# Performance work log

Hardware: AMD Instinct MI355X
Metric: run time of the kernel (lower is better)

The kernel has to match this reference:

```python
import jax, jax.numpy as jnp
import numpy as np
import math

DIM = 2048
NUM_HEADS = 16
HEAD_DIM = 128
SEQ = 2048
BATCH = 2
THETA = 10000.0


def _rope_freqs(seq_len, head_dim, theta=THETA):
    half = head_dim // 2
    inv = 1.0 / (theta ** (np.arange(0, half, dtype=np.float32) / half))
    t = np.arange(seq_len, dtype=np.float32)
    ang = np.outer(t, inv)  # [S, half]
    return jnp.asarray(np.cos(ang)), jnp.asarray(np.sin(ang))


def setup_inputs() -> dict:
    key = jax.random.key(0)
    ks = jax.random.split(key, 5)
    s = 1.0 / math.sqrt(DIM)
    cos, sin = _rope_freqs(SEQ, HEAD_DIM)
    return {
        "x": jax.random.normal(ks[0], (BATCH, SEQ, DIM), dtype=jnp.float32),
        "wq": jax.random.normal(ks[1], (DIM, NUM_HEADS * HEAD_DIM), dtype=jnp.float32) * s,
        "wk": jax.random.normal(ks[2], (DIM, NUM_HEADS * HEAD_DIM), dtype=jnp.float32) * s,
        "wv": jax.random.normal(ks[3], (DIM, NUM_HEADS * HEAD_DIM), dtype=jnp.float32) * s,
        "wo": jax.random.normal(ks[4], (NUM_HEADS * HEAD_DIM, DIM), dtype=jnp.float32) * s,
        "freqs_cos": cos,
        "freqs_sin": sin,
    }


def _apply_rope(x, cos, sin):
    # x: [B, S, H, Hd]; cos/sin: [S, Hd//2]
    B, S, H, Hd = x.shape
    xr = x.astype(jnp.float32).reshape(B, S, H, Hd // 2, 2)
    x0, x1 = xr[..., 0], xr[..., 1]
    c = cos[:S][None, :, None, :]
    sn = sin[:S][None, :, None, :]
    o0 = x0 * c - x1 * sn
    o1 = x0 * sn + x1 * c
    return jnp.stack([o0, o1], axis=-1).reshape(B, S, H, Hd)


def reference(x, wq, wk, wv, wo, freqs_cos, freqs_sin):
    B, S, D = x.shape
    H, Hd = NUM_HEADS, HEAD_DIM
    q = (x @ wq).reshape(B, S, H, Hd)
    k = (x @ wk).reshape(B, S, H, Hd)
    v = (x @ wv).reshape(B, S, H, Hd)
    q = _apply_rope(q, freqs_cos, freqs_sin)
    k = _apply_rope(k, freqs_cos, freqs_sin)
    # [B, H, S, S] causal attention scores
    scores = jnp.einsum("bqhd,bkhd->bhqk", q, k) / math.sqrt(Hd)
    causal = jnp.tril(jnp.ones((S, S), dtype=bool))
    scores = jnp.where(causal[None, None], scores, -jnp.inf)
    probs = jax.nn.softmax(scores.astype(jnp.float32), axis=-1)
    o = jnp.einsum("bhqk,bkhd->bqhd", probs, v).reshape(B, S, H * Hd)
    return o @ wo
```

## Files before the change

### kernel.cpp

```cpp
#include <hip/hip_runtime.h>
#include <hip/hip_bf16.h>

typedef __bf16 bf16;
typedef __attribute__((ext_vector_type(8))) __bf16 bf16x8;
typedef __attribute__((ext_vector_type(4))) __bf16 bf16x4;
typedef __attribute__((ext_vector_type(4))) float  f32x4;

typedef const void __attribute__((address_space(1)))* gas_t;
typedef void __attribute__((address_space(3)))* las_t;

__device__ __forceinline__ void gload16(const void* g, void* l) {
  __builtin_amdgcn_global_load_lds((gas_t)g, (las_t)l, 16, 0, 0);
}
__device__ __forceinline__ f32x4 mfma16(bf16x8 a, bf16x8 b, f32x4 c) {
  return __builtin_amdgcn_mfma_f32_16x16x32_bf16(a, b, c, 0, 0, 0);
}

constexpr int SEQL = 2048;
constexpr int DM   = 2048;
constexpr int HD   = 128;
constexpr int MR   = 4096;

__global__ __launch_bounds__(256) void cvt_x(const float* __restrict__ x,
                                             bf16* __restrict__ xb) {
  const size_t i = ((size_t)blockIdx.x * 256 + threadIdx.x) * 4;
  const f32x4 v = *reinterpret_cast<const f32x4*>(x + i);
  bf16x4 o;
  #pragma unroll
  for (int j = 0; j < 4; ++j) o[j] = (bf16)v[j];
  *reinterpret_cast<bf16x4*>(xb + i) = o;
}

__global__ __launch_bounds__(256) void transpose_w(
    const float* __restrict__ w0, const float* __restrict__ w1,
    const float* __restrict__ w2, const float* __restrict__ w3,
    bf16* __restrict__ wqkvt, bf16* __restrict__ wot) {
  const int z = blockIdx.z;
  const float* src = (z == 0) ? w0 : (z == 1) ? w1 : (z == 2) ? w2 : w3;
  bf16* dst = (z < 3) ? (wqkvt + (size_t)z * DM * DM) : wot;
  __shared__ float tile[32][33];
  const int tx = threadIdx.x, ty = threadIdx.y;
  const int x0 = blockIdx.x * 32, y0 = blockIdx.y * 32;
  #pragma unroll
  for (int i = 0; i < 4; ++i)
    tile[ty + 8 * i][tx] = src[(size_t)(y0 + ty + 8 * i) * DM + x0 + tx];
  __syncthreads();
  #pragma unroll
  for (int i = 0; i < 4; ++i)
    dst[(size_t)(x0 + ty + 8 * i) * DM + y0 + tx] = (bf16)tile[tx][ty + 8 * i];
}

__global__ __launch_bounds__(256) void rope_k(bf16* __restrict__ Q,
                                              bf16* __restrict__ Kk,
                                              const float* __restrict__ fc,
                                              const float* __restrict__ fs) {
  bf16* X = blockIdx.y ? Kk : Q;
  const size_t tid = (size_t)blockIdx.x * 256 + threadIdx.x;
  const size_t e0 = tid * 8;
  const int col = (int)(e0 & (DM - 1));
  const int row = (int)(e0 >> 11);
  const int s   = row & (SEQL - 1);
  const int p0  = (col & (HD - 1)) >> 1;
  bf16x8 v = *reinterpret_cast<bf16x8*>(X + e0);
  const f32x4 c  = *reinterpret_cast<const f32x4*>(fc + (size_t)s * 64 + p0);
  const f32x4 sn = *reinterpret_cast<const f32x4*>(fs + (size_t)s * 64 + p0);
  #pragma unroll
  for (int j = 0; j < 4; ++j) {
    const float x0 = (float)v[2 * j], x1 = (float)v[2 * j + 1];
    v[2 * j]     = (bf16)(x0 * c[j] - x1 * sn[j]);
    v[2 * j + 1] = (bf16)(x0 * sn[j] + x1 * c[j]);
  }
  *reinterpret_cast<bf16x8*>(X + e0) = v;
}

#define GPH(Q, STAGE, TAIL)                                                    \
  {                                                                            \
    const char* ap = aB + ((Q) * 32 + lo) * 128;                               \
    const bf16x8 a00 = *(const bf16x8*)(ap + su0);                             \
    const bf16x8 a01 = *(const bf16x8*)(ap + su1);                             \
    const bf16x8 a10 = *(const bf16x8*)(ap + 2048 + su0);                      \
    const bf16x8 a11 = *(const bf16x8*)(ap + 2048 + su1);                      \
    STAGE                                                                      \
    __builtin_amdgcn_s_barrier();                                              \
    asm volatile("s_waitcnt lgkmcnt(0)" ::: "memory");                         \
    __builtin_amdgcn_s_setprio(1);                                             \
    _Pragma("unroll")                                                          \
    for (int nf = 0; nf < 4; ++nf) {                                           \
      acc[2 * (Q)][nf]     = mfma16(a00, bfr[nf][0], acc[2 * (Q)][nf]);        \
      acc[2 * (Q)][nf]     = mfma16(a01, bfr[nf][1], acc[2 * (Q)][nf]);        \
      acc[2 * (Q) + 1][nf] = mfma16(a10, bfr[nf][0], acc[2 * (Q) + 1][nf]);    \
      acc[2 * (Q) + 1][nf] = mfma16(a11, bfr[nf][1], acc[2 * (Q) + 1][nf]);    \
    }                                                                          \
    __builtin_amdgcn_s_setprio(0);                                             \
    TAIL                                                                       \
    __builtin_amdgcn_s_barrier();                                              \
    asm volatile("" ::: "memory");                                             \
  }

template <bool MULTI>
__global__ __launch_bounds__(512, 2) void gemm8(
    const bf16* __restrict__ A, const bf16* __restrict__ Bt,
    bf16* __restrict__ Cb, const int M, const int N, const int K) {
  __shared__ __attribute__((aligned(16))) char lds[131072];
  const int t = threadIdx.x;
  const int wid = t >> 6, lane = t & 63, lo = lane & 15, hi = lane >> 4;
  const int wm = wid >> 2, wn = wid & 3;

  const int bid = blockIdx.x;
  const int nx = bid & 7;
  const int my = MULTI ? ((bid >> 3) & 15) : (bid >> 3);
  const int z  = MULTI ? (bid >> 7) : 0;
  const int m0 = my * 256, n0 = nx * 256;
  const bf16* Bt_ = Bt + (MULTI ? (size_t)z * N * K : 0);
  bf16* Cb_ = Cb + (MULTI ? (size_t)z * M * N : 0);

  const int urow  = (wid << 3) + (lane >> 3);
  const int uunit = (lane & 7) ^ ((lane >> 3) & 7);
  const bf16* gA = A   + (size_t)(m0 + urow) * K + uunit * 8;
  const bf16* gB = Bt_ + (size_t)(n0 + urow) * K + uunit * 8;
  char* lw = lds + wid * 1024;

  const int NT = K >> 6;

  auto stg = [&](const bf16* gbase, int buf, int op, int h, int kt) {
    const bf16* g = gbase + (size_t)(h * 128) * K + kt * 64;
    char* l = lw + (((buf << 1) | op) * 2 + h) * 16384;
    gload16(g, l);
    gload16(g + (size_t)64 * K, l + 8192);
  };
  auto stB0 = [&](int kt2) { stg(gB, kt2 & 1, 1, 0, kt2); };
  auto stB1 = [&](int kt2) { stg(gB, kt2 & 1, 1, 1, kt2); };
  auto stA0 = [&](int kt2) { stg(gA, kt2 & 1, 0, 0, kt2); };
  auto stA1 = [&](int kt2) { stg(gA, kt2 & 1, 0, 1, kt2); };

  f32x4 acc[8][4];
  #pragma unroll
  for (int i = 0; i < 8; ++i)
    #pragma unroll
    for (int j = 0; j < 4; ++j) acc[i][j] = (f32x4){0.f, 0.f, 0.f, 0.f};

  const int su0 = (hi ^ (lo & 7)) * 16;
  const int su1 = ((4 + hi) ^ (lo & 7)) * 16;

  stB0(0); stB1(0); stA0(0); stA1(0);
  stB0(1); stB1(1); stA0(1);
  asm volatile("s_waitcnt vmcnt(6)" ::: "memory");
  __builtin_amdgcn_s_barrier();
  asm volatile("" ::: "memory");

  #pragma unroll 1
  for (int kt = 0; kt < NT; ++kt) {
    const int bufc = kt & 1;
    const char* aB = lds + ((bufc * 2 + 0) * 2 + wm) * 16384;
    const char* bB = lds + ((bufc * 2 + 1) * 2 + (wn >> 1)) * 16384;
    bf16x8 bfr[4][2];
    {
      const char* bp = bB + ((wn & 1) * 64 + lo) * 128;
      #pragma unroll
      for (int nf = 0; nf < 4; ++nf) {
        bfr[nf][0] = *(const bf16x8*)(bp + nf * 2048 + su0);
        bfr[nf][1] = *(const bf16x8*)(bp + nf * 2048 + su1);
      }
    }
    GPH(0, if (kt + 1 < NT) stA1(kt + 1);, )
    GPH(1, if (kt + 2 < NT) stB0(kt + 2);, )
    GPH(2, if (kt + 2 < NT) stB1(kt + 2);, )
    GPH(3, if (kt + 2 < NT) stA0(kt + 2);,
        if (kt + 2 < NT) { asm volatile("s_waitcnt vmcnt(6)" ::: "memory"); }
        else             { asm volatile("s_waitcnt vmcnt(0)" ::: "memory"); })
  }

  #pragma unroll
  for (int mf = 0; mf < 8; ++mf)
    #pragma unroll
    for (int nf = 0; nf < 4; ++nf)
      #pragma unroll
      for (int r = 0; r < 4; ++r) {
        const size_t row = m0 + wm * 128 + mf * 16 + hi * 4 + r;
        const size_t col = n0 + wn * 64 + nf * 16 + lo;
        Cb_[row * N + col] = (bf16)acc[mf][nf][r];
      }
}

__global__ __launch_bounds__(256) void gemm_bt_f32(
    const bf16* __restrict__ A, const bf16* __restrict__ Bt,
    float* __restrict__ Cf, const int M, const int N, const int K) {
  const int t = threadIdx.x;
  const int wid = t >> 6, lane = t & 63, lo = lane & 15, hi = lane >> 4;
  const int m0 = blockIdx.y * 128, n0 = blockIdx.x * 128;
  __shared__ bf16 As[128 * 32];
  __shared__ bf16 Bs[128 * 32];
  const int wr = wid >> 1, wc = wid & 1;
  const f32x4 zero4 = {0.f, 0.f, 0.f, 0.f};
  f32x4 acc[4][4];
  #pragma unroll
  for (int i = 0; i < 4; ++i)
    #pragma unroll
    for (int j = 0; j < 4; ++j) acc[i][j] = zero4;

  const int r_a = t >> 2;
  const int ul  = ((t & 3) ^ (r_a & 3)) * 8;
  const bf16* gA0 = A  + (size_t)(m0 + r_a) * K + ul;
  const bf16* gB0 = Bt + (size_t)(n0 + r_a) * K + ul;
  char* lA = (char*)As + wid * 1024;
  char* lB = (char*)Bs + wid * 1024;

  const int ru = (hi ^ (lo & 3)) * 8;

  for (int k0 = 0; k0 < K; k0 += 32) {
    gload16(gA0 + k0, lA);
    gload16(gA0 + (size_t)64 * K + k0, lA + 4096);
    gload16(gB0 + k0, lB);
    gload16(gB0 + (size_t)64 * K + k0, lB + 4096);
    __syncthreads();
    bf16x8 af[4], bb[4];
    #pragma unroll
    for (int i = 0; i < 4; ++i)
      af[i] = *reinterpret_cast<const bf16x8*>(As + (wr * 64 + i * 16 + lo) * 32 + ru);
    #pragma unroll
    for (int i = 0; i < 4; ++i)
      bb[i] = *reinterpret_cast<const bf16x8*>(Bs + (wc * 64 + i * 16 + lo) * 32 + ru);
    #pragma unroll
    for (int mi = 0; mi < 4; ++mi)
      #pragma unroll
      for (int ni = 0; ni < 4; ++ni)
        acc[mi][ni] = mfma16(af[mi], bb[ni], acc[mi][ni]);
    __syncthreads();
  }
  #pragma unroll
  for (int mi = 0; mi < 4; ++mi)
    #pragma unroll
    for (int ni = 0; ni < 4; ++ni)
      #pragma unroll
      for (int r = 0; r < 4; ++r) {
        const size_t row = m0 + wr * 64 + mi * 16 + hi * 4 + r;
        const size_t col = n0 + wc * 64 + ni * 16 + lo;
        Cf[row * N + col] = acc[mi][ni][r];
      }
}

__global__ __launch_bounds__(256) void flash_fwd(
    const bf16* __restrict__ Qg, const bf16* __restrict__ Kg,
    const bf16* __restrict__ Vg, bf16* __restrict__ Og) {
  const int t = threadIdx.x;
  const int wid = t >> 6, lane = t & 63, lo = lane & 15, hi = lane >> 4;
  const int h  = blockIdx.y;
  const int b  = blockIdx.z;

  __shared__ bf16 Ks[64 * 128];
  __shared__ bf16 Vt[128 * 64];
  __shared__ bf16 Ps[4][16 * 64];

  const size_t hoff = (size_t)b * SEQL * DM + (size_t)h * HD;
  const float SCALE_LOG2 = 0.12751743f;

  const int krow = t >> 4;
  const int kul  = ((t & 15) ^ krow) * 8;
  const int vd0  = (t & 31) * 4;
  const int vg   = t >> 5;
  char* myP = (char*)(Ps[wid]);
  const f32x4 zero4 = {0.f, 0.f, 0.f, 0.f};

  #pragma unroll 1
  for (int pass = 0; pass < 2; ++pass) {
    const int q0 = (pass ? (31 - (int)blockIdx.x) : (int)blockIdx.x) * 64;

    bf16x8 qf[4];
    {
      const bf16* qrow = Qg + hoff + (size_t)(q0 + wid * 16 + lo) * DM;
      #pragma unroll
      for (int kc = 0; kc < 4; ++kc)
        qf[kc] = *reinterpret_cast<const bf16x8*>(qrow + kc * 32 + hi * 8);
    }

    f32x4 acc[8];
    #pragma unroll
    for (int i = 0; i < 8; ++i) acc[i] = zero4;
    float m_run = -1e30f, l_run = 0.f;

    const int ntiles = q0 / 64 + 1;
    #pragma unroll 1
    for (int it = 0; it < ntiles; ++it) {
      const int kv0 = it * 64;
      {
        const bf16* gK = Kg + hoff + (size_t)(kv0 + krow) * DM + kul;
        char* lK = (char*)Ks + wid * 1024;
        #pragma unroll
        for (int j = 0; j < 4; ++j)
          gload16(gK + (size_t)j * 16 * DM, lK + j * 4096);
      }
      {
        const bf16* gV = Vg + hoff + (size_t)kv0 * DM + vd0;
        bf16x4 ld[8];
        #pragma unroll
        for (int e = 0; e < 8; ++e)
          ld[e] = *reinterpret_cast<const bf16x4*>(gV + (size_t)(vg * 8 + e) * DM);
        #pragma unroll
        for (int c = 0; c < 4; ++c) {
          const int d = vd0 + c;
          const int sw = (d ^ (d >> 3)) & 7;
          bf16x8 pk;
          #pragma unroll
          for (int e = 0; e < 8; ++e) pk[e] = ld[e][c];
          *reinterpret_cast<bf16x8*>(Vt + d * 64 + ((vg ^ sw) * 8)) = pk;
        }
      }
      __syncthreads();

      f32x4 s[4];
      #pragma unroll
      for (int nf = 0; nf < 4; ++nf) s[nf] = zero4;
      #pragma unroll
      for (int nf = 0; nf < 4; ++nf) {
        const bf16* krp = Ks + (nf * 16 + lo) * 128;
        #pragma unroll
        for (int kc = 0; kc < 4; ++kc) {
          const bf16x8 kb = *reinterpret_cast<const bf16x8*>(krp + (((kc * 4 + hi) ^ lo) * 8));
          s[nf] = mfma16(kb, qf[kc], s[nf]);
        }
      }
      const bool boundary = (kv0 == q0);
      #pragma unroll
      for (int nf = 0; nf < 4; ++nf)
        #pragma unroll
        for (int r = 0; r < 4; ++r) {
          float v = s[nf][r] * SCALE_LOG2;
          if (boundary && (nf * 16 + hi * 4 + r > wid * 16 + lo)) v = -1e30f;
          s[nf][r] = v;
        }
      float pmax = -1e30f;
      #pragma unroll
      for (int nf = 0; nf < 4; ++nf)
        #pragma unroll
        for (int r = 0; r < 4; ++r) pmax = fmaxf(pmax, s[nf][r]);
      pmax = fmaxf(pmax, __shfl_xor(pmax, 16, 64));
      pmax = fmaxf(pmax, __shfl_xor(pmax, 32, 64));
      float mnew = m_run;
      if (!__all(pmax <= m_run)) {
        mnew = fmaxf(m_run, pmax);
        const float fctr = exp2f(m_run - mnew);
        m_run = mnew;
        l_run *= fctr;
        float fa[4];
        #pragma unroll
        for (int r = 0; r < 4; ++r) fa[r] = __shfl(fctr, hi * 4 + r, 64);
        #pragma unroll
        for (int i = 0; i < 8; ++i)
          #pragma unroll
          for (int r = 0; r < 4; ++r) acc[i][r] *= fa[r];
      }
      float sum = 0.f;
      #pragma unroll
      for (int nf = 0; nf < 4; ++nf)
        #pragma unroll
        for (int r = 0; r < 4; ++r) {
          const float p = exp2f(s[nf][r] - mnew);
          s[nf][r] = p;
          sum += p;
        }
      sum += __shfl_xor(sum, 16, 64);
      sum += __shfl_xor(sum, 32, 64);
      l_run += sum;
      #pragma unroll
      for (int nf = 0; nf < 4; ++nf) {
        bf16x4 w;
        #pragma unroll
        for (int r = 0; r < 4; ++r) w[r] = (bf16)s[nf][r];
        *reinterpret_cast<bf16x4*>(myP + lo * 128 +
            (((nf * 2 + (hi >> 1)) ^ (lo & 7)) * 16) + (hi & 1) * 8) = w;
      }
      bf16x8 pa[2];
      #pragma unroll
      for (int kc = 0; kc < 2; ++kc)
        pa[kc] = *reinterpret_cast<const bf16x8*>(myP + lo * 128 +
            (((kc * 4 + hi) ^ (lo & 7)) * 16));
      #pragma unroll
      for (int nf = 0; nf < 8; ++nf) {
        const int d = nf * 16 + lo;
        const int sw = (d ^ (d >> 3)) & 7;
        const bf16* vrp = Vt + d * 64;
        #pragma unroll
        for (int kc = 0; kc < 2; ++kc) {
          const bf16x8 bv = *reinterpret_cast<const bf16x8*>(vrp + (((kc * 4 + hi) ^ sw) * 8));
          acc[nf] = mfma16(pa[kc], bv, acc[nf]);
        }
      }
      __syncthreads();
    }

    const float linv = 1.f / l_run;
    float la[4];
    #pragma unroll
    for (int r = 0; r < 4; ++r) la[r] = __shfl(linv, hi * 4 + r, 64);
    #pragma unroll
    for (int nf = 0; nf < 8; ++nf)
      #pragma unroll
      for (int r = 0; r < 4; ++r) {
        const size_t row = q0 + wid * 16 + hi * 4 + r;
        Og[hoff + row * DM + nf * 16 + lo] = (bf16)(acc[nf][r] * la[r]);
      }
  }
}

extern "C" void kernel_launch(void* const* d_in, const int* in_sizes, int n_in,
                              void* d_out, int out_size, void* d_ws, size_t ws_size,
                              hipStream_t stream) {
  const float* x  = (const float*)d_in[0];
  const float* wq = (const float*)d_in[1];
  const float* wk = (const float*)d_in[2];
  const float* wv = (const float*)d_in[3];
  const float* wo = (const float*)d_in[4];
  const float* fc = (const float*)d_in[5];
  const float* fs = (const float*)d_in[6];
  float* out = (float*)d_out;

  char* ws = (char*)d_ws;
  bf16* xb    = (bf16*)ws;
  bf16* wqkvt = (bf16*)(ws + (16ull << 20));
  bf16* wot   = (bf16*)(ws + (40ull << 20));
  bf16* qkv   = (bf16*)(ws + (48ull << 20));
  bf16* Qb = qkv;
  bf16* Kb = qkv + (size_t)MR * DM;
  bf16* Vb = qkv + 2 * (size_t)MR * DM;

  cvt_x<<<8192, 256, 0, stream>>>(x, xb);
  transpose_w<<<dim3(64, 64, 4), dim3(32, 8), 0, stream>>>(wq, wk, wv, wo, wqkvt, wot);
  gemm8<true><<<384, 512, 0, stream>>>(xb, wqkvt, qkv, MR, DM, DM);
  rope_k<<<dim3(4096, 2), 256, 0, stream>>>(Qb, Kb, fc, fs);
  flash_fwd<<<dim3(16, 16, 2), 256, 0, stream>>>(Qb, Kb, Vb, xb );
  gemm_bt_f32<<<dim3(16, 32), 256, 0, stream>>>(xb, wot, out, MR, DM, DM);
}
```

Measured before the change: 423.8 us.

## Software-pipeline A fragments in QKV GEMM, remap blocks per XCD, widen flash tiles

The QKV GEMM now double-buffers A-operand register fragments so the LDS reads for the next quarter overlap the current MFMAs. It issues the A prefetch for k+2 together and remaps block IDs so each XCD owns adjacent M rows, aiming for better L2 reuse. Flash attention moves to 512-thread blocks covering 128 query rows with a per-wave causal mask, which halves the number of K/V tile loads per query row. The cost is more barriers and registers in the GEMM, and longer causal-boundary handling in the attention kernel.

```diff
diff --git a/kernel.cpp b/kernel.cpp
--- a/kernel.cpp
+++ b/kernel.cpp
@@ -15,6 +15,8 @@
 __device__ __forceinline__ f32x4 mfma16(bf16x8 a, bf16x8 b, f32x4 c) {
   return __builtin_amdgcn_mfma_f32_16x16x32_bf16(a, b, c, 0, 0, 0);
 }
+#define BARRIER() do { asm volatile("" ::: "memory"); \
+  __builtin_amdgcn_s_barrier(); asm volatile("" ::: "memory"); } while (0)
 
 constexpr int SEQL = 2048;
 constexpr int DM   = 2048;
@@ -73,31 +75,27 @@
   *reinterpret_cast<bf16x8*>(X + e0) = v;
 }
 
-#define GPH(Q, STAGE, TAIL)                                                    \
+#define LDA4(DST, BASE, ROWOFF)                                                \
   {                                                                            \
-    const char* ap = aB + ((Q) * 32 + lo) * 128;                               \
-    const bf16x8 a00 = *(const bf16x8*)(ap + su0);                             \
-    const bf16x8 a01 = *(const bf16x8*)(ap + su1);                             \
-    const bf16x8 a10 = *(const bf16x8*)(ap + 2048 + su0);                      \
-    const bf16x8 a11 = *(const bf16x8*)(ap + 2048 + su1);                      \
-    STAGE                                                                      \
-    __builtin_amdgcn_s_barrier();                                              \
-    asm volatile("s_waitcnt lgkmcnt(0)" ::: "memory");                         \
+    const char* ap_ = (BASE) + ((ROWOFF) + lo) * 128;                          \
+    DST[0] = *(const bf16x8*)(ap_ + su0);                                      \
+    DST[1] = *(const bf16x8*)(ap_ + su1);                                      \
+    DST[2] = *(const bf16x8*)(ap_ + 2048 + su0);                               \
+    DST[3] = *(const bf16x8*)(ap_ + 2048 + su1);                               \
+  }
+#define MFMAQ(Q, AR)                                                           \
+  {                                                                            \
     __builtin_amdgcn_s_setprio(1);                                             \
     _Pragma("unroll")                                                          \
     for (int nf = 0; nf < 4; ++nf) {                                           \
-      acc[2 * (Q)][nf]     = mfma16(a00, bfr[nf][0], acc[2 * (Q)][nf]);        \
-      acc[2 * (Q)][nf]     = mfma16(a01, bfr[nf][1], acc[2 * (Q)][nf]);        \
-      acc[2 * (Q) + 1][nf] = mfma16(a10, bfr[nf][0], acc[2 * (Q) + 1][nf]);    \
-      acc[2 * (Q) + 1][nf] = mfma16(a11, bfr[nf][1], acc[2 * (Q) + 1][nf]);    \
+      acc[2 * (Q)][nf]     = mfma16(AR[0], bfr[nf][0], acc[2 * (Q)][nf]);      \
+      acc[2 * (Q)][nf]     = mfma16(AR[1], bfr[nf][1], acc[2 * (Q)][nf]);      \
+      acc[2 * (Q) + 1][nf] = mfma16(AR[2], bfr[nf][0], acc[2 * (Q) + 1][nf]);  \
+      acc[2 * (Q) + 1][nf] = mfma16(AR[3], bfr[nf][1], acc[2 * (Q) + 1][nf]);  \
     }                                                                          \
     __builtin_amdgcn_s_setprio(0);                                             \
-    TAIL                                                                       \
-    __builtin_amdgcn_s_barrier();                                              \
-    asm volatile("" ::: "memory");                                             \
-  }
-
-template <bool MULTI>
+  }
+
 __global__ __launch_bounds__(512, 2) void gemm8(
     const bf16* __restrict__ A, const bf16* __restrict__ Bt,
     bf16* __restrict__ Cb, const int M, const int N, const int K) {
@@ -107,19 +105,19 @@
   const int wm = wid >> 2, wn = wid & 3;
 
   const int bid = blockIdx.x;
-  const int nx = bid & 7;
-  const int my = MULTI ? ((bid >> 3) & 15) : (bid >> 3);
-  const int z  = MULTI ? (bid >> 7) : 0;
+  const int xcd = bid & 7, idx = bid >> 3;
+  const int my = (xcd << 1) | (idx & 1);
+  const int nxz = idx >> 1;
+  const int nx = nxz & 7, z = nxz >> 3;
   const int m0 = my * 256, n0 = nx * 256;
-  const bf16* Bt_ = Bt + (MULTI ? (size_t)z * N * K : 0);
-  bf16* Cb_ = Cb + (MULTI ? (size_t)z * M * N : 0);
+  const bf16* Bt_ = Bt + (size_t)z * N * K;
+  bf16* Cb_ = Cb + (size_t)z * M * N;
 
   const int urow  = (wid << 3) + (lane >> 3);
   const int uunit = (lane & 7) ^ ((lane >> 3) & 7);
   const bf16* gA = A   + (size_t)(m0 + urow) * K + uunit * 8;
   const bf16* gB = Bt_ + (size_t)(n0 + urow) * K + uunit * 8;
   char* lw = lds + wid * 1024;
-
   const int NT = K >> 6;
 
   auto stg = [&](const bf16* gbase, int buf, int op, int h, int kt) {
@@ -128,10 +126,10 @@
     gload16(g, l);
     gload16(g + (size_t)64 * K, l + 8192);
   };
-  auto stB0 = [&](int kt2) { stg(gB, kt2 & 1, 1, 0, kt2); };
-  auto stB1 = [&](int kt2) { stg(gB, kt2 & 1, 1, 1, kt2); };
-  auto stA0 = [&](int kt2) { stg(gA, kt2 & 1, 0, 0, kt2); };
-  auto stA1 = [&](int kt2) { stg(gA, kt2 & 1, 0, 1, kt2); };
+  auto stB0 = [&](int k2) { stg(gB, k2 & 1, 1, 0, k2); };
+  auto stB1 = [&](int k2) { stg(gB, k2 & 1, 1, 1, k2); };
+  auto stA0 = [&](int k2) { stg(gA, k2 & 1, 0, 0, k2); };
+  auto stA1 = [&](int k2) { stg(gA, k2 & 1, 0, 1, k2); };
 
   f32x4 acc[8][4];
   #pragma unroll
@@ -143,16 +141,19 @@
   const int su1 = ((4 + hi) ^ (lo & 7)) * 16;
 
   stB0(0); stB1(0); stA0(0); stA1(0);
-  stB0(1); stB1(1); stA0(1);
-  asm volatile("s_waitcnt vmcnt(6)" ::: "memory");
-  __builtin_amdgcn_s_barrier();
-  asm volatile("" ::: "memory");
+  stB0(1); stB1(1); stA0(1); stA1(1);
+  asm volatile("s_waitcnt vmcnt(8)" ::: "memory");
+  BARRIER();
+
+  bf16x8 aP0[4], aP1[4];
+  LDA4(aP0, lds + wm * 16384, 0);
 
   #pragma unroll 1
   for (int kt = 0; kt < NT; ++kt) {
-    const int bufc = kt & 1;
-    const char* aB = lds + ((bufc * 2 + 0) * 2 + wm) * 16384;
-    const char* bB = lds + ((bufc * 2 + 1) * 2 + (wn >> 1)) * 16384;
+    const int bc = kt & 1;
+    const char* aB = lds + (bc * 4 + wm) * 16384;
+    const char* bB = lds + ((bc * 2 + 1) * 2 + (wn >> 1)) * 16384;
+    const char* aN = lds + (((kt + 1) & 1) * 4 + wm) * 16384;
     bf16x8 bfr[4][2];
     {
       const char* bp = bB + ((wn & 1) * 64 + lo) * 128;
@@ -162,12 +163,27 @@
         bfr[nf][1] = *(const bf16x8*)(bp + nf * 2048 + su1);
       }
     }
-    GPH(0, if (kt + 1 < NT) stA1(kt + 1);, )
-    GPH(1, if (kt + 2 < NT) stB0(kt + 2);, )
-    GPH(2, if (kt + 2 < NT) stB1(kt + 2);, )
-    GPH(3, if (kt + 2 < NT) stA0(kt + 2);,
-        if (kt + 2 < NT) { asm volatile("s_waitcnt vmcnt(6)" ::: "memory"); }
-        else             { asm volatile("s_waitcnt vmcnt(0)" ::: "memory"); })
+    LDA4(aP1, aB, 32);
+    BARRIER();
+    MFMAQ(0, aP0)
+    BARRIER();
+    LDA4(aP0, aB, 64);
+    if (kt + 2 < NT) stB0(kt + 2);
+    BARRIER();
+    MFMAQ(1, aP1)
+    BARRIER();
+    LDA4(aP1, aB, 96);
+    if (kt + 2 < NT) stB1(kt + 2);
+    BARRIER();
+    MFMAQ(2, aP0)
+    BARRIER();
+    if (kt + 2 < NT)      { asm volatile("s_waitcnt vmcnt(4)" ::: "memory"); }
+    else if (kt + 1 < NT) { asm volatile("s_waitcnt vmcnt(0)" ::: "memory"); }
+    BARRIER();
+    if (kt + 1 < NT) LDA4(aP0, aN, 0);
+    if (kt + 2 < NT) { stA0(kt + 2); stA1(kt + 2); }
+    MFMAQ(3, aP1)
+    BARRIER();
   }
 
   #pragma unroll
@@ -239,7 +255,7 @@
       }
 }
 
-__global__ __launch_bounds__(256) void flash_fwd(
+__global__ __launch_bounds__(512) void flash_fwd(
     const bf16* __restrict__ Qg, const bf16* __restrict__ Kg,
     const bf16* __restrict__ Vg, bf16* __restrict__ Og) {
   const int t = threadIdx.x;
@@ -249,21 +265,21 @@
 
   __shared__ bf16 Ks[64 * 128];
   __shared__ bf16 Vt[128 * 64];
-  __shared__ bf16 Ps[4][16 * 64];
+  __shared__ bf16 Ps[8][16 * 64];
 
   const size_t hoff = (size_t)b * SEQL * DM + (size_t)h * HD;
   const float SCALE_LOG2 = 0.12751743f;
 
   const int krow = t >> 4;
-  const int kul  = ((t & 15) ^ krow) * 8;
+  const int kul  = ((t & 15) ^ (krow & 15)) * 8;
   const int vd0  = (t & 31) * 4;
-  const int vg   = t >> 5;
+  const int vg   = (t >> 5) & 15;
   char* myP = (char*)(Ps[wid]);
   const f32x4 zero4 = {0.f, 0.f, 0.f, 0.f};
 
   #pragma unroll 1
   for (int pass = 0; pass < 2; ++pass) {
-    const int q0 = (pass ? (31 - (int)blockIdx.x) : (int)blockIdx.x) * 64;
+    const int q0 = (pass ? (15 - (int)blockIdx.x) : (int)blockIdx.x) * 128;
 
     bf16x8 qf[4];
     {
@@ -278,31 +294,31 @@
     for (int i = 0; i < 8; ++i) acc[i] = zero4;
     float m_run = -1e30f, l_run = 0.f;
 
-    const int ntiles = q0 / 64 + 1;
+    const int ntiles = q0 / 64 + 2;
     #pragma unroll 1
     for (int it = 0; it < ntiles; ++it) {
       const int kv0 = it * 64;
       {
         const bf16* gK = Kg + hoff + (size_t)(kv0 + krow) * DM + kul;
         char* lK = (char*)Ks + wid * 1024;
-        #pragma unroll
-        for (int j = 0; j < 4; ++j)
-          gload16(gK + (size_t)j * 16 * DM, lK + j * 4096);
+        gload16(gK, lK);
+        gload16(gK + (size_t)32 * DM, lK + 8192);
       }
       {
-        const bf16* gV = Vg + hoff + (size_t)kv0 * DM + vd0;
-        bf16x4 ld[8];
-        #pragma unroll
-        for (int e = 0; e < 8; ++e)
-          ld[e] = *reinterpret_cast<const bf16x4*>(gV + (size_t)(vg * 8 + e) * DM);
+        const bf16* gV = Vg + hoff + (size_t)(kv0 + vg * 4) * DM + vd0;
+        bf16x4 ld[4];
+        #pragma unroll
+        for (int e = 0; e < 4; ++e)
+          ld[e] = *reinterpret_cast<const bf16x4*>(gV + (size_t)e * DM);
         #pragma unroll
         for (int c = 0; c < 4; ++c) {
           const int d = vd0 + c;
           const int sw = (d ^ (d >> 3)) & 7;
-          bf16x8 pk;
+          bf16x4 w;
           #pragma unroll
-          for (int e = 0; e < 8; ++e) pk[e] = ld[e][c];
-          *reinterpret_cast<bf16x8*>(Vt + d * 64 + ((vg ^ sw) * 8)) = pk;
+          for (int e = 0; e < 4; ++e) w[e] = ld[e][c];
+          *reinterpret_cast<bf16x4*>(Vt + d * 64 + (((vg >> 1) ^ sw) * 8) +
+                                     (vg & 1) * 4) = w;
         }
       }
       __syncthreads();
@@ -319,13 +335,13 @@
           s[nf] = mfma16(kb, qf[kc], s[nf]);
         }
       }
-      const bool boundary = (kv0 == q0);
+      const bool boundary = (kv0 + 63 > q0 + wid * 16);
       #pragma unroll
       for (int nf = 0; nf < 4; ++nf)
         #pragma unroll
         for (int r = 0; r < 4; ++r) {
           float v = s[nf][r] * SCALE_LOG2;
-          if (boundary && (nf * 16 + hi * 4 + r > wid * 16 + lo)) v = -1e30f;
+          if (boundary && (kv0 + nf * 16 + hi * 4 + r > q0 + wid * 16 + lo)) v = -1e30f;
           s[nf][r] = v;
         }
       float pmax = -1e30f;
@@ -425,8 +441,8 @@
 
   cvt_x<<<8192, 256, 0, stream>>>(x, xb);
   transpose_w<<<dim3(64, 64, 4), dim3(32, 8), 0, stream>>>(wq, wk, wv, wo, wqkvt, wot);
-  gemm8<true><<<384, 512, 0, stream>>>(xb, wqkvt, qkv, MR, DM, DM);
+  gemm8<<<384, 512, 0, stream>>>(xb, wqkvt, qkv, MR, DM, DM);
   rope_k<<<dim3(4096, 2), 256, 0, stream>>>(Qb, Kb, fc, fs);
-  flash_fwd<<<dim3(16, 16, 2), 256, 0, stream>>>(Qb, Kb, Vb, xb );
+  flash_fwd<<<dim3(8, 16, 2), 512, 0, stream>>>(Qb, Kb, Vb, xb );
   gemm_bt_f32<<<dim3(16, 32), 256, 0, stream>>>(xb, wot, out, MR, DM, DM);
 }
```

Result: no change. 419.0 us (-1.1%).
